# Kernel optimization log

Hardware: AMD Instinct MI355X
Metric: run time of the kernel (lower is better)

The kernel has to match this reference:

```python
import jax, jax.numpy as jnp
import numpy as np

B, S, D, H = 4, 2048, 1024, 16
HD = D // H  # head dim = 64


def setup_inputs() -> dict:
    key = jax.random.key(0)
    ks = jax.random.split(key, 5)
    scale = 1.0 / np.sqrt(D)
    return {
        "X": jax.random.normal(ks[0], (B, S, D), dtype=jnp.float32),
        "Wq": jax.random.normal(ks[1], (D, D), dtype=jnp.float32) * scale,
        "Wk": jax.random.normal(ks[2], (D, D), dtype=jnp.float32) * scale,
        "Wv": jax.random.normal(ks[3], (D, D), dtype=jnp.float32) * scale,
        "Wo": jax.random.normal(ks[4], (D, D), dtype=jnp.float32) * scale,
    }


def _split_heads(x):
    # [B, S, D] -> [B, H, S, HD]
    b, s, d = x.shape
    return x.reshape(b, s, H, HD).transpose(0, 2, 1, 3)


def reference(X, Wq, Wk, Wv, Wo):
    q = _split_heads(X @ Wq)  # [B, H, S, HD]
    k = _split_heads(X @ Wk)
    v = _split_heads(X @ Wv)
    scores = jnp.einsum("bhqd,bhkd->bhqk", q, k) / jnp.sqrt(jnp.float32(HD))
    causal = jnp.tril(jnp.ones((S, S), dtype=bool))  # [S, S]
    scores = jnp.where(causal[None, None, :, :], scores, jnp.float32(-jnp.inf))
    attn = jax.nn.softmax(scores, axis=-1)
    out = jnp.einsum("bhqk,bhkd->bhqd", attn, v)  # [B, H, S, HD]
    out = out.transpose(0, 2, 1, 3).reshape(B, S, D)  # merge heads
    return out @ Wo
```

## Files before the change

kernel.cpp:

```cpp
#include <hip/hip_runtime.h>
#include <hip/hip_bf16.h>

typedef __attribute__((ext_vector_type(8))) short short8;
typedef __attribute__((ext_vector_type(8))) unsigned short ushort8;
typedef __attribute__((ext_vector_type(4))) unsigned short bf16x4;
typedef __attribute__((ext_vector_type(4))) float f32x4;

#define BDIM 1024
#define SEQ  2048
#define NHD  16
#define NEGBIG (-1.0e30f)

__device__ __forceinline__ unsigned short f2bf(float x) {
  union { __hip_bfloat16 h; unsigned short u; } cv;
  cv.h = __float2bfloat16(x);
  return cv.u;
}

__device__ __forceinline__ void gload16(const void* g, void* l) {
  __builtin_amdgcn_global_load_lds((const __attribute__((address_space(1))) void*)g,
                                   (__attribute__((address_space(3))) void*)l, 16, 0, 0);
}

__global__ __launch_bounds__(256) void cvt_f32_bf16(const float* __restrict__ src,
                                                    unsigned short* __restrict__ dst) {
  int i = (blockIdx.x * 256 + threadIdx.x) * 8;
  float4 a = *(const float4*)(src + i);
  float4 b = *(const float4*)(src + i + 4);
  ushort8 o;
  o[0] = f2bf(a.x); o[1] = f2bf(a.y); o[2] = f2bf(a.z); o[3] = f2bf(a.w);
  o[4] = f2bf(b.x); o[5] = f2bf(b.y); o[6] = f2bf(b.z); o[7] = f2bf(b.w);
  *(ushort8*)(dst + i) = o;
}

__global__ __launch_bounds__(256) void wtrans(const float* __restrict__ src,
                                              unsigned short* __restrict__ dst) {
  __shared__ float t[32][33];
  int tx = threadIdx.x, ty = threadIdx.y;
  int c0 = blockIdx.x * 32, r0 = blockIdx.y * 32;
  for (int i = ty; i < 32; i += 8)
    t[i][tx] = src[(size_t)(r0 + i) * BDIM + c0 + tx];
  __syncthreads();
  for (int i = ty; i < 32; i += 8)
    dst[(size_t)(c0 + i) * BDIM + r0 + tx] = f2bf(t[tx][i]);
}

template <bool F32OUT>
__global__ __launch_bounds__(256) void gemm_bt(const unsigned short* __restrict__ A,
                                               const unsigned short* __restrict__ BT,
                                               void* __restrict__ Cv) {
  __shared__ __align__(16) unsigned short As[128 * 64];
  __shared__ __align__(16) unsigned short Bs[128 * 64];
  const int tid = threadIdx.x;
  const int lane = tid & 63;
  const int w = tid >> 6;
  const int wr = w >> 1, wc = w & 1;
  const int m0 = blockIdx.x * 128;
  const int n0 = blockIdx.y * 128;
  const int l15 = lane & 15, lg = lane >> 4;

  f32x4 acc[4][4] = {};

  for (int k0 = 0; k0 < BDIM; k0 += 64) {
    for (int j = 0; j < 4; ++j) {
      int ob = (w * 4 + j) * 1024;
      int o = ob + lane * 16;
      int row = o >> 7;
      int kb = (o & 127) ^ ((row & 7) << 4);
      gload16(A + (size_t)(m0 + row) * BDIM + k0 + (kb >> 1), (char*)As + ob);
      gload16(BT + (size_t)(n0 + row) * BDIM + k0 + (kb >> 1), (char*)Bs + ob);
    }
    __syncthreads();
    for (int ks = 0; ks < 64; ks += 32) {
      int kb = (ks + lg * 8) * 2;
      short8 a[4], b[4];
      for (int mi = 0; mi < 4; ++mi) {
        int row = wr * 64 + mi * 16 + l15;
        a[mi] = *(const short8*)((const char*)As + row * 128 + (kb ^ ((row & 7) << 4)));
      }
      for (int nj = 0; nj < 4; ++nj) {
        int row = wc * 64 + nj * 16 + l15;
        b[nj] = *(const short8*)((const char*)Bs + row * 128 + (kb ^ ((row & 7) << 4)));
      }
      for (int mi = 0; mi < 4; ++mi)
        for (int nj = 0; nj < 4; ++nj)
          acc[mi][nj] = __builtin_amdgcn_mfma_f32_16x16x32_bf16(a[mi], b[nj], acc[mi][nj], 0, 0, 0);
    }
    __syncthreads();
  }
  for (int mi = 0; mi < 4; ++mi)
    for (int nj = 0; nj < 4; ++nj) {
      int m = m0 + wr * 64 + mi * 16 + lg * 4;
      int n = n0 + wc * 64 + nj * 16 + l15;
      for (int r = 0; r < 4; ++r) {
        if constexpr (F32OUT)
          ((float*)Cv)[(size_t)(m + r) * BDIM + n] = acc[mi][nj][r];
        else
          ((unsigned short*)Cv)[(size_t)(m + r) * BDIM + n] = f2bf(acc[mi][nj][r]);
      }
    }
}

__global__ __launch_bounds__(512) void attn(const unsigned short* __restrict__ Qg,
                                            const unsigned short* __restrict__ Kg,
                                            const unsigned short* __restrict__ Vg,
                                            unsigned short* __restrict__ Og) {
  __shared__ __align__(16) unsigned short Ks[2][64 * 64];
  __shared__ __align__(16) unsigned short VTs[2][64 * 64];
  __shared__ __align__(16) unsigned short Ps[128 * 64];

  const int tid = threadIdx.x;
  const int lane = tid & 63;
  const int w = tid >> 6;
  const int l15 = lane & 15, lg = lane >> 4;
  const int bh = blockIdx.x;
  const size_t base = ((size_t)(bh >> 4) * SEQ) * BDIM + (size_t)(bh & 15) * 64;
  constexpr float C = 0.125f * 1.44269504089f;

  const int srow = tid >> 3;
  const int scol = (((tid & 7) * 16) ^ ((srow & 7) << 4)) >> 1;
  const int sdst = tid * 16;
  const int vp = tid & 31, vd = tid >> 5;
  int vdst[4];
  for (int e = 0; e < 4; ++e) {
    int d = vd * 4 + e;
    vdst[e] = d * 128 + ((4 * vp) ^ ((((d & 7) ^ (d >> 3)) & 7) << 4));
  }

  for (int half = 0; half < 2; ++half) {
    const int c = half == 0 ? (int)blockIdx.y : 15 - (int)blockIdx.y;
    const int q0 = c * 128;

    gload16(Qg + base + (size_t)(q0 + srow) * BDIM + scol, (char*)Ps + sdst);
    gload16(Qg + base + (size_t)(q0 + 64 + srow) * BDIM + scol, (char*)Ps + 8192 + sdst);
    __syncthreads();
    short8 qf[2];
    {
      int row = w * 16 + l15;
      int sz = (row & 7) << 4;
      qf[0] = *(const short8*)((const char*)Ps + row * 128 + ((lg * 16) ^ sz));
      qf[1] = *(const short8*)((const char*)Ps + row * 128 + ((64 + lg * 16) ^ sz));
    }

    float mrow = NEGBIG, lrow = 0.f;
    f32x4 oacc[4] = {};

    const int ntiles = 2 * c + 2;

    bf16x4 v0, v1;
    gload16(Kg + base + (size_t)(srow) * BDIM + scol, (char*)Ks[0] + sdst);
    {
      const unsigned short* vs = Vg + base + (size_t)(2 * vp) * BDIM + vd * 4;
      v0 = *(const bf16x4*)vs;
      v1 = *(const bf16x4*)(vs + BDIM);
    }
    for (int e = 0; e < 4; ++e) {
      unsigned int pk = (unsigned int)v0[e] | ((unsigned int)v1[e] << 16);
      *(unsigned int*)((char*)VTs[0] + vdst[e]) = pk;
    }
    __syncthreads();

    int cur = 0;
    for (int t = 0; t < ntiles; ++t) {
      const int kv0 = t * 64;
      const bool more = (t + 1 < ntiles);
      if (more) {
        const int nv0 = kv0 + 64;
        gload16(Kg + base + (size_t)(nv0 + srow) * BDIM + scol, (char*)Ks[cur ^ 1] + sdst);
        const unsigned short* vs = Vg + base + (size_t)(nv0 + 2 * vp) * BDIM + vd * 4;
        v0 = *(const bf16x4*)vs;
        v1 = *(const bf16x4*)(vs + BDIM);
      }

      if (kv0 <= q0 + w * 16 + 15) {
        f32x4 s2[4];
        for (int kvj = 0; kvj < 4; ++kvj) {
          int row = kvj * 16 + l15;
          int sz = (row & 7) << 4;
          short8 kf0 = *(const short8*)((const char*)Ks[cur] + row * 128 + ((lg * 16) ^ sz));
          short8 kf1 = *(const short8*)((const char*)Ks[cur] + row * 128 + ((64 + lg * 16) ^ sz));
          f32x4 z = {};
          z = __builtin_amdgcn_mfma_f32_16x16x32_bf16(kf0, qf[0], z, 0, 0, 0);
          z = __builtin_amdgcn_mfma_f32_16x16x32_bf16(kf1, qf[1], z, 0, 0, 0);
          s2[kvj] = z;
        }
        const int qbase = q0 + w * 16;
        const int qc = qbase + l15;
        float mx = NEGBIG;
        if (kv0 + 63 > qbase) {
          for (int kvj = 0; kvj < 4; ++kvj)
            for (int r = 0; r < 4; ++r) {
              int kv = kv0 + kvj * 16 + 4 * lg + r;
              float v = s2[kvj][r];
              if (kv > qc) { v = NEGBIG; s2[kvj][r] = v; }
              mx = fmaxf(mx, v);
            }
        } else {
          for (int kvj = 0; kvj < 4; ++kvj)
            for (int r = 0; r < 4; ++r) mx = fmaxf(mx, s2[kvj][r]);
        }
        mx = fmaxf(mx, __shfl_xor(mx, 16));
        mx = fmaxf(mx, __shfl_xor(mx, 32));
        if (!__all(mx <= mrow)) {
          float mnew = fmaxf(mrow, mx);
          float sc = __builtin_amdgcn_exp2f((mrow - mnew) * C);
          mrow = mnew;
          lrow *= sc;
          for (int di = 0; di < 4; ++di)
            for (int r = 0; r < 4; ++r) oacc[di][r] *= sc;
        }
        const float mC = mrow * C;
        float rs = 0.f;
        for (int kvj = 0; kvj < 4; ++kvj)
          for (int r = 0; r < 4; ++r) {
            float p = __builtin_amdgcn_exp2f(fmaf(s2[kvj][r], C, -mC));
            s2[kvj][r] = p;
            rs += p;
          }
        rs += __shfl_xor(rs, 16);
        rs += __shfl_xor(rs, 32);
        lrow += rs;
        int prow = w * 16 + l15;
        int psz = (prow & 7) << 4;
        for (int kvj = 0; kvj < 4; ++kvj) {
          bf16x4 pk;
          pk[0] = f2bf(s2[kvj][0]); pk[1] = f2bf(s2[kvj][1]);
          pk[2] = f2bf(s2[kvj][2]); pk[3] = f2bf(s2[kvj][3]);
          *(bf16x4*)((char*)Ps + prow * 128 + ((kvj * 32 + lg * 8) ^ psz)) = pk;
        }
        for (int ks = 0; ks < 2; ++ks) {
          short8 pa = *(const short8*)((const char*)Ps + prow * 128 +
                                       ((ks * 64 + lg * 16) ^ psz));
          for (int di = 0; di < 4; ++di) {
            int d = di * 16 + l15;
            short8 vf = *(const short8*)((const char*)VTs[cur] + d * 128 +
                                         ((ks * 64 + lg * 16) ^ ((((d & 7) ^ (d >> 3)) & 7) << 4)));
            oacc[di] = __builtin_amdgcn_mfma_f32_16x16x32_bf16(vf, pa, oacc[di], 0, 0, 0);
          }
        }
      }

      if (more) {
        for (int e = 0; e < 4; ++e) {
          unsigned int pk = (unsigned int)v0[e] | ((unsigned int)v1[e] << 16);
          *(unsigned int*)((char*)VTs[cur ^ 1] + vdst[e]) = pk;
        }
      }
      __syncthreads();
      cur ^= 1;
    }

    {
      float inv = 1.0f / lrow;
      int qrow = q0 + w * 16 + l15;
      for (int di = 0; di < 4; ++di) {
        bf16x4 ov;
        for (int r = 0; r < 4; ++r) ov[r] = f2bf(oacc[di][r] * inv);
        *(bf16x4*)(Og + base + (size_t)qrow * BDIM + di * 16 + 4 * lg) = ov;
      }
    }
  }
}

extern "C" void kernel_launch(void* const* d_in, const int* in_sizes, int n_in,
                              void* d_out, int out_size, void* d_ws, size_t ws_size,
                              hipStream_t stream) {
  const float* X  = (const float*)d_in[0];
  const float* Wq = (const float*)d_in[1];
  const float* Wk = (const float*)d_in[2];
  const float* Wv = (const float*)d_in[3];
  const float* Wo = (const float*)d_in[4];

  const size_t WSZ = (size_t)1024 * 1024;
  const size_t MSZ = (size_t)8192 * 1024;
  const size_t need = (4 * WSZ + 4 * MSZ) * 2;
  if (ws_size < need) return;

  unsigned short* ws = (unsigned short*)d_ws;
  unsigned short* WqT = ws;
  unsigned short* WkT = WqT + WSZ;
  unsigned short* WvT = WkT + WSZ;
  unsigned short* WoT = WvT + WSZ;
  unsigned short* Qw  = WoT + WSZ;
  unsigned short* Kw  = Qw + MSZ;
  unsigned short* Vw  = Kw + MSZ;
  unsigned short* Ow  = Vw + MSZ;
  unsigned short* Xb  = (unsigned short*)d_out;

  dim3 tb(32, 8);
  dim3 tg(32, 32);
  wtrans<<<tg, tb, 0, stream>>>(Wq, WqT);
  wtrans<<<tg, tb, 0, stream>>>(Wk, WkT);
  wtrans<<<tg, tb, 0, stream>>>(Wv, WvT);
  wtrans<<<tg, tb, 0, stream>>>(Wo, WoT);

  cvt_f32_bf16<<<(8192 * 1024) / (256 * 8), 256, 0, stream>>>(X, Xb);

  dim3 gg(64, 8);
  gemm_bt<false><<<gg, 256, 0, stream>>>(Xb, WqT, Qw);
  gemm_bt<false><<<gg, 256, 0, stream>>>(Xb, WkT, Kw);
  gemm_bt<false><<<gg, 256, 0, stream>>>(Xb, WvT, Vw);

  attn<<<dim3(64, 8), 512, 0, stream>>>(Qw, Kw, Vw, Ow);

  gemm_bt<true><<<gg, 256, 0, stream>>>(Ow, WoT, d_out);
}
```

Before: 194.2 us.

## Double-buffer GEMM LDS tiles and batch QKV and weight-transpose launches

The GEMM main loop now uses two LDS buffers per operand and issues the global-to-LDS loads for the next K tile before computing on the current one, which drops one barrier per iteration and overlaps loads with MFMA work. The three Q/K/V projection GEMMs are merged into one launch using blockIdx.z, and the four weight transposes are merged the same way. This removes launch overhead and gives the QKV GEMM three times as many blocks. In exchange, LDS use per block doubles to 64KB, which can lower occupancy.

```diff
diff --git a/kernel.cpp b/kernel.cpp
--- a/kernel.cpp
+++ b/kernel.cpp
@@ -33,8 +33,12 @@
   *(ushort8*)(dst + i) = o;
 }
 
-__global__ __launch_bounds__(256) void wtrans(const float* __restrict__ src,
-                                              unsigned short* __restrict__ dst) {
+__global__ __launch_bounds__(256) void wtrans4(const float* __restrict__ s0, const float* __restrict__ s1,
+                                               const float* __restrict__ s2, const float* __restrict__ s3,
+                                               unsigned short* __restrict__ d0, unsigned short* __restrict__ d1,
+                                               unsigned short* __restrict__ d2, unsigned short* __restrict__ d3) {
+  const float* src = blockIdx.z == 0 ? s0 : blockIdx.z == 1 ? s1 : blockIdx.z == 2 ? s2 : s3;
+  unsigned short* dst = blockIdx.z == 0 ? d0 : blockIdx.z == 1 ? d1 : blockIdx.z == 2 ? d2 : d3;
   __shared__ float t[32][33];
   int tx = threadIdx.x, ty = threadIdx.y;
   int c0 = blockIdx.x * 32, r0 = blockIdx.y * 32;
@@ -46,11 +50,10 @@
 }
 
 template <bool F32OUT>
-__global__ __launch_bounds__(256) void gemm_bt(const unsigned short* __restrict__ A,
-                                               const unsigned short* __restrict__ BT,
-                                               void* __restrict__ Cv) {
-  __shared__ __align__(16) unsigned short As[128 * 64];
-  __shared__ __align__(16) unsigned short Bs[128 * 64];
+__device__ __forceinline__ void gemm_body(const unsigned short* __restrict__ A,
+                                          const unsigned short* __restrict__ BT,
+                                          void* __restrict__ Cv,
+                                          unsigned short* As, unsigned short* Bs) {
   const int tid = threadIdx.x;
   const int lane = tid & 63;
   const int w = tid >> 6;
@@ -59,35 +62,53 @@
   const int n0 = blockIdx.y * 128;
   const int l15 = lane & 15, lg = lane >> 4;
 
+  int ob[4], grow[4], gcol[4];
+  for (int j = 0; j < 4; ++j) {
+    ob[j] = (w * 4 + j) * 1024;
+    int o = ob[j] + lane * 16;
+    int row = o >> 7;
+    int kb = (o & 127) ^ ((row & 7) << 4);
+    grow[j] = row; gcol[j] = kb >> 1;
+  }
+
   f32x4 acc[4][4] = {};
 
+  for (int j = 0; j < 4; ++j) {
+    gload16(A + (size_t)(m0 + grow[j]) * BDIM + gcol[j], (char*)As + ob[j]);
+    gload16(BT + (size_t)(n0 + grow[j]) * BDIM + gcol[j], (char*)Bs + ob[j]);
+  }
+  __syncthreads();
+
+  int cur = 0;
   for (int k0 = 0; k0 < BDIM; k0 += 64) {
-    for (int j = 0; j < 4; ++j) {
-      int ob = (w * 4 + j) * 1024;
-      int o = ob + lane * 16;
-      int row = o >> 7;
-      int kb = (o & 127) ^ ((row & 7) << 4);
-      gload16(A + (size_t)(m0 + row) * BDIM + k0 + (kb >> 1), (char*)As + ob);
-      gload16(BT + (size_t)(n0 + row) * BDIM + k0 + (kb >> 1), (char*)Bs + ob);
-    }
-    __syncthreads();
+    if (k0 + 64 < BDIM) {
+      int nb = (cur ^ 1) * 16384;
+      for (int j = 0; j < 4; ++j) {
+        gload16(A + (size_t)(m0 + grow[j]) * BDIM + (k0 + 64) + gcol[j], (char*)As + nb + ob[j]);
+        gload16(BT + (size_t)(n0 + grow[j]) * BDIM + (k0 + 64) + gcol[j], (char*)Bs + nb + ob[j]);
+      }
+    }
+    const char* Ab = (const char*)As + cur * 16384;
+    const char* Bb = (const char*)Bs + cur * 16384;
     for (int ks = 0; ks < 64; ks += 32) {
       int kb = (ks + lg * 8) * 2;
       short8 a[4], b[4];
       for (int mi = 0; mi < 4; ++mi) {
         int row = wr * 64 + mi * 16 + l15;
-        a[mi] = *(const short8*)((const char*)As + row * 128 + (kb ^ ((row & 7) << 4)));
+        a[mi] = *(const short8*)(Ab + row * 128 + (kb ^ ((row & 7) << 4)));
       }
       for (int nj = 0; nj < 4; ++nj) {
         int row = wc * 64 + nj * 16 + l15;
-        b[nj] = *(const short8*)((const char*)Bs + row * 128 + (kb ^ ((row & 7) << 4)));
+        b[nj] = *(const short8*)(Bb + row * 128 + (kb ^ ((row & 7) << 4)));
       }
       for (int mi = 0; mi < 4; ++mi)
         for (int nj = 0; nj < 4; ++nj)
           acc[mi][nj] = __builtin_amdgcn_mfma_f32_16x16x32_bf16(a[mi], b[nj], acc[mi][nj], 0, 0, 0);
     }
     __syncthreads();
-  }
+    cur ^= 1;
+  }
+
   for (int mi = 0; mi < 4; ++mi)
     for (int nj = 0; nj < 4; ++nj) {
       int m = m0 + wr * 64 + mi * 16 + lg * 4;
@@ -99,6 +120,29 @@
           ((unsigned short*)Cv)[(size_t)(m + r) * BDIM + n] = f2bf(acc[mi][nj][r]);
       }
     }
+}
+
+__global__ __launch_bounds__(256) void gemm_qkv(const unsigned short* __restrict__ A,
+                                                const unsigned short* __restrict__ B0,
+                                                const unsigned short* __restrict__ B1,
+                                                const unsigned short* __restrict__ B2,
+                                                unsigned short* __restrict__ C0,
+                                                unsigned short* __restrict__ C1,
+                                                unsigned short* __restrict__ C2) {
+  __shared__ __align__(16) unsigned short As[2 * 128 * 64];
+  __shared__ __align__(16) unsigned short Bs[2 * 128 * 64];
+  const unsigned short* BT = blockIdx.z == 0 ? B0 : blockIdx.z == 1 ? B1 : B2;
+  unsigned short* C = blockIdx.z == 0 ? C0 : blockIdx.z == 1 ? C1 : C2;
+  gemm_body<false>(A, BT, C, As, Bs);
+}
+
+template <bool F32OUT>
+__global__ __launch_bounds__(256) void gemm_bt(const unsigned short* __restrict__ A,
+                                               const unsigned short* __restrict__ BT,
+                                               void* __restrict__ Cv) {
+  __shared__ __align__(16) unsigned short As[2 * 128 * 64];
+  __shared__ __align__(16) unsigned short Bs[2 * 128 * 64];
+  gemm_body<F32OUT>(A, BT, Cv, As, Bs);
 }
 
 __global__ __launch_bounds__(512) void attn(const unsigned short* __restrict__ Qg,
@@ -287,21 +331,13 @@
   unsigned short* Ow  = Vw + MSZ;
   unsigned short* Xb  = (unsigned short*)d_out;
 
-  dim3 tb(32, 8);
-  dim3 tg(32, 32);
-  wtrans<<<tg, tb, 0, stream>>>(Wq, WqT);
-  wtrans<<<tg, tb, 0, stream>>>(Wk, WkT);
-  wtrans<<<tg, tb, 0, stream>>>(Wv, WvT);
-  wtrans<<<tg, tb, 0, stream>>>(Wo, WoT);
+  wtrans4<<<dim3(32, 32, 4), dim3(32, 8), 0, stream>>>(Wq, Wk, Wv, Wo, WqT, WkT, WvT, WoT);
 
   cvt_f32_bf16<<<(8192 * 1024) / (256 * 8), 256, 0, stream>>>(X, Xb);
 
-  dim3 gg(64, 8);
-  gemm_bt<false><<<gg, 256, 0, stream>>>(Xb, WqT, Qw);
-  gemm_bt<false><<<gg, 256, 0, stream>>>(Xb, WkT, Kw);
-  gemm_bt<false><<<gg, 256, 0, stream>>>(Xb, WvT, Vw);
+  gemm_qkv<<<dim3(64, 8, 3), 256, 0, stream>>>(Xb, WqT, WkT, WvT, Qw, Kw, Vw);
 
   attn<<<dim3(64, 8), 512, 0, stream>>>(Qw, Kw, Vw, Ow);
 
-  gemm_bt<true><<<gg, 256, 0, stream>>>(Ow, WoT, d_out);
-}
+  gemm_bt<true><<<dim3(64, 8), 256, 0, stream>>>(Ow, WoT, d_out);
+}
```

Result: faster. 170.5 us (-12.2%).
